# Performance work log

Measured on AMD Instinct MI355X. Metric: run time of the kernel, lower is better.

The kernel has to match this reference:

```python
import jax, jax.numpy as jnp
import numpy as np

DIM, N_HEAD, N_KV, HEAD_DIM = 4096, 32, 8, 128
B, S = 2, 2048


def apply_rotary_emb(x, freqs_cis):
    # x: [B, S, H, D]; freqs_cis: [S, D//2, 2]
    xs = x.reshape(x.shape[:-1] + (-1, 2))            # [B,S,H,D/2,2]
    f = freqs_cis.reshape(1, xs.shape[1], 1, xs.shape[3], 2)
    x0, x1 = xs[..., 0], xs[..., 1]
    f0, f1 = f[..., 0], f[..., 1]
    out = jnp.stack([x0 * f0 - x1 * f1, x0 * f1 + x1 * f0], axis=-1)
    return out.reshape(x.shape).astype(x.dtype)


def setup_inputs() -> dict:
    key = jax.random.key(0)
    k1, k2, k3, k4 = jax.random.split(key, 4)
    x = jax.random.normal(k1, (B, S, DIM), dtype=jnp.float32)
    freqs_cis = jax.random.normal(k2, (S, HEAD_DIM // 2, 2), dtype=jnp.float32)
    # causal boolean mask (True = attend)
    mask_cache = jnp.tril(jnp.ones((S, S), dtype=bool))[None, None]
    input_pos = jnp.arange(S, dtype=jnp.int32)
    total_head_dim = (N_HEAD + 2 * N_KV) * HEAD_DIM
    wqkv = jax.random.normal(k3, (total_head_dim, DIM), dtype=jnp.float32) * (DIM ** -0.5)
    wo = jax.random.normal(k4, (DIM, DIM), dtype=jnp.float32) * (DIM ** -0.5)
    return {"x": x, "freqs_cis": freqs_cis, "mask_cache": mask_cache,
            "input_pos": input_pos, "wqkv": wqkv, "wo": wo}


def reference(x, freqs_cis, mask_cache, input_pos, wqkv, wo):
    bsz, seqlen, _ = x.shape
    kv_size = N_KV * HEAD_DIM
    qkv = jnp.einsum('bsd,fd->bsf', x, wqkv)
    q, k, v = jnp.split(qkv, [DIM, DIM + kv_size], axis=-1)
    q = q.reshape(bsz, seqlen, N_HEAD, HEAD_DIM)
    k = k.reshape(bsz, seqlen, N_KV, HEAD_DIM)
    v = v.reshape(bsz, seqlen, N_KV, HEAD_DIM)
    q = apply_rotary_emb(q, freqs_cis)
    k = apply_rotary_emb(k, freqs_cis)
    q = q.transpose(0, 2, 1, 3)   # [B,Hq,S,D]
    k = k.transpose(0, 2, 1, 3)   # [B,Hkv,S,D]
    v = v.transpose(0, 2, 1, 3)
    # GQA: repeat kv heads to match query heads
    g = N_HEAD // N_KV
    k = jnp.repeat(k, g, axis=1)
    v = jnp.repeat(v, g, axis=1)
    scale = 1.0 / jnp.sqrt(jnp.asarray(HEAD_DIM, dtype=q.dtype))
    scores = jnp.einsum('bhqd,bhkd->bhqk', q, k) * scale
    neg_inf = jnp.asarray(jnp.finfo(scores.dtype).min, dtype=scores.dtype)
    scores = jnp.where(mask_cache, scores, neg_inf)
    attn = jax.nn.softmax(scores, axis=-1)
    y = jnp.einsum('bhqk,bhkd->bhqd', attn, v)
    y = y.transpose(0, 2, 1, 3).reshape(bsz, seqlen, DIM)
    return jnp.einsum('bsd,od->bso', y, wo)
```

## Files before the change

kernel.cpp:

```cpp
#include <hip/hip_runtime.h>
#include <hip/hip_bf16.h>

#define DIM   4096
#define NHEAD 32
#define NKV   8
#define HD    128
#define BATCH 2
#define SEQ   2048
#define M1    (BATCH*SEQ)
#define NF    ((NHEAD+2*NKV)*HD)

typedef __attribute__((ext_vector_type(8))) short short8;
typedef __attribute__((ext_vector_type(4))) short short4v;
typedef __attribute__((ext_vector_type(4))) float f32x4;

__device__ __forceinline__ float bf2f(short s) {
    unsigned u = ((unsigned)(unsigned short)s) << 16;
    return __builtin_bit_cast(float, u);
}
__device__ __forceinline__ short f2bf(float f) {
    unsigned u = __builtin_bit_cast(unsigned, f);
    u = u + 0x7fffu + ((u >> 16) & 1u);
    return (short)(u >> 16);
}

__device__ __forceinline__ void gload_lds16(const void* g, void* l) {
    __builtin_amdgcn_global_load_lds(
        (const __attribute__((address_space(1))) void*)g,
        (__attribute__((address_space(3))) void*)l, 16, 0, 0);
}

__global__ void f2bf2_k(const float* __restrict__ a, short* __restrict__ da, int na8,
                        const float* __restrict__ b, short* __restrict__ db, int nb8) {
    const int total = na8 + nb8;
    const int stride = gridDim.x * blockDim.x;
    for (int i = blockIdx.x * blockDim.x + threadIdx.x; i < total; i += stride) {
        const float* s; short* d; int j = i;
        if (j < na8) { s = a; d = da; }
        else         { j -= na8; s = b; d = db; }
        float4 v0 = ((const float4*)s)[2*j];
        float4 v1 = ((const float4*)s)[2*j + 1];
        short8 o;
        o[0] = f2bf(v0.x); o[1] = f2bf(v0.y); o[2] = f2bf(v0.z); o[3] = f2bf(v0.w);
        o[4] = f2bf(v1.x); o[5] = f2bf(v1.y); o[6] = f2bf(v1.z); o[7] = f2bf(v1.w);
        ((short8*)d)[j] = o;
    }
}
__global__ void f2bf_k(const float* __restrict__ src, short* __restrict__ dst, int n8) {
    const int stride = gridDim.x * blockDim.x;
    for (int i = blockIdx.x * blockDim.x + threadIdx.x; i < n8; i += stride) {
        float4 v0 = ((const float4*)src)[2*i];
        float4 v1 = ((const float4*)src)[2*i + 1];
        short8 o;
        o[0] = f2bf(v0.x); o[1] = f2bf(v0.y); o[2] = f2bf(v0.z); o[3] = f2bf(v0.w);
        o[4] = f2bf(v1.x); o[5] = f2bf(v1.y); o[6] = f2bf(v1.z); o[7] = f2bf(v1.w);
        ((short8*)dst)[i] = o;
    }
}

template<int OUT_BF16>
__global__ __launch_bounds__(512, 2) void gemm256(const short* __restrict__ A,
                                                  const short* __restrict__ Bm,
                                                  void* __restrict__ Cout,
                                                  int M, int N, int K) {
    __shared__ __align__(16) short As[2][2][128*64];
    __shared__ __align__(16) short Bs[2][2][128*64];
    const int nbn = N >> 8;
    const int nwg = gridDim.x;
    const int cpx = nwg >> 3;
    const int swz = (blockIdx.x & 7) * cpx + (blockIdx.x >> 3);
    const int brow = swz / nbn, bcol = swz % nbn;
    const int t = threadIdx.x, lane = t & 63, w = t >> 6;
    const int wm = w >> 2, wn = w & 3;
    const int l16 = lane & 15, lhi = lane >> 4, l7 = l16 & 7;
    const size_t abase = (size_t)brow * 256 * K;
    const size_t bbase = (size_t)bcol * 256 * K;
    const int sr = t >> 3;
    const int sc = t & 7;
    const int scl = sc ^ (sr & 7);
    f32x4 acc[8][4] = {};

    auto stageA = [&](int kt, int qm) {
#pragma unroll
        for (int i = 0; i < 2; ++i)
            gload_lds16(A + abase + (size_t)(i*128 + qm*64 + sr) * K + kt*64 + scl*8,
                        &As[kt & 1][qm][(i*64 + sr)*64 + sc*8]);
    };
    auto stageB = [&](int kt, int qn) {
#pragma unroll
        for (int i = 0; i < 2; ++i)
            gload_lds16(Bm + bbase + (size_t)((i*2 + (sr>>5))*64 + qn*32 + (sr & 31)) * K + kt*64 + scl*8,
                        &Bs[kt & 1][qn][(i*64 + sr)*64 + sc*8]);
    };

    const int NT = K >> 6;
    stageA(0, 0); stageB(0, 0); stageA(0, 1); stageB(0, 1);
    stageA(1, 0); stageB(1, 0);
    asm volatile("s_waitcnt vmcnt(4)" ::: "memory");
    __builtin_amdgcn_s_barrier();

    short8 a0[4][2], a1[4][2], b0[2][2], b1[2][2];

#define LD_A(dst, P, QM)                                                        \
    _Pragma("unroll") for (int mi = 0; mi < 4; ++mi)                            \
    _Pragma("unroll") for (int kk = 0; kk < 2; ++kk)                            \
        dst[mi][kk] = *(const short8*)&As[P][QM][(wm*64 + mi*16 + l16)*64 + (((kk*4 + lhi) ^ l7) * 8)];
#define LD_B(dst, P, QN)                                                        \
    _Pragma("unroll") for (int ni = 0; ni < 2; ++ni)                            \
    _Pragma("unroll") for (int kk = 0; kk < 2; ++kk)                            \
        dst[ni][kk] = *(const short8*)&Bs[P][QN][(wn*32 + ni*16 + l16)*64 + (((kk*4 + lhi) ^ l7) * 8)];
#define MMA(QM, QN, af, bf)                                                     \
    __builtin_amdgcn_s_barrier();                                               \
    __builtin_amdgcn_s_setprio(1);                                              \
    _Pragma("unroll") for (int kk = 0; kk < 2; ++kk)                            \
    _Pragma("unroll") for (int mi = 0; mi < 4; ++mi)                            \
    _Pragma("unroll") for (int ni = 0; ni < 2; ++ni)                            \
        acc[QM*4 + mi][QN*2 + ni] = __builtin_amdgcn_mfma_f32_16x16x32_bf16(    \
            af[mi][kk], bf[ni][kk], acc[QM*4 + mi][QN*2 + ni], 0, 0, 0);        \
    __builtin_amdgcn_s_setprio(0);

    LD_A(a0, 0, 0)
    LD_B(b0, 0, 0)

    for (int cur = 0; cur < NT; ++cur) {
        const int d = cur & 1, dn = d ^ 1;
        LD_B(b1, d, 1)
        if (cur + 1 < NT) stageA(cur + 1, 1);
        MMA(0, 0, a0, b0)
        asm volatile("s_waitcnt vmcnt(2)" ::: "memory");
        LD_A(a1, d, 1)
        if (cur + 1 < NT) stageB(cur + 1, 1);
        MMA(0, 1, a0, b1)
        LD_A(a0, dn, 0)
        if (cur + 2 < NT) stageA(cur + 2, 0);
        MMA(1, 0, a1, b0)
        if (cur + 2 < NT) { asm volatile("s_waitcnt vmcnt(2)" ::: "memory"); }
        else              { asm volatile("s_waitcnt vmcnt(0)" ::: "memory"); }
        LD_B(b0, dn, 0)
        if (cur + 2 < NT) stageB(cur + 2, 0);
        MMA(1, 1, a1, b1)
    }
#undef LD_A
#undef LD_B
#undef MMA

#pragma unroll
    for (int fm = 0; fm < 8; ++fm)
#pragma unroll
        for (int fn = 0; fn < 4; ++fn)
#pragma unroll
            for (int r = 0; r < 4; ++r) {
                size_t row = (size_t)brow*256 + wm*128 + fm*16 + lhi*4 + r;
                size_t col = (size_t)bcol*256 + wn*64 + fn*16 + l16;
                if (OUT_BF16)
                    ((short*)Cout)[row * N + col] = f2bf(acc[fm][fn][r]);
                else
                    ((float*)Cout)[row * N + col] = acc[fm][fn][r];
            }
}

__global__ void rope_split_k(const short* __restrict__ qkv,
                             const float* __restrict__ freqs,
                             short* __restrict__ qb, short* __restrict__ kb) {
    int tid  = blockIdx.x * blockDim.x + threadIdx.x;
    int colg = tid % 640;
    int row  = tid / 640;
    if (row >= M1) return;
    int b = row >> 11, s = row & 2047;
    int f = colg << 3;
    int h = f >> 7, d = f & 127;
    short8 v = *(const short8*)&qkv[(size_t)row * NF + f];
    const float4 fa = *(const float4*)&freqs[(size_t)(s*64 + (d>>1)) * 2];
    const float4 fb = *(const float4*)&freqs[(size_t)(s*64 + (d>>1)) * 2 + 4];
    float fr[8] = {fa.x, fa.y, fa.z, fa.w, fb.x, fb.y, fb.z, fb.w};
    short8 o;
#pragma unroll
    for (int p = 0; p < 4; ++p) {
        float x0 = bf2f(v[2*p]), x1 = bf2f(v[2*p+1]);
        float c = fr[2*p], sn = fr[2*p+1];
        o[2*p]   = f2bf(x0 * c  - x1 * sn);
        o[2*p+1] = f2bf(x0 * sn + x1 * c);
    }
    if (h < NHEAD)
        *(short8*)&qb[((((size_t)b*NHEAD + h)*SEQ + s) << 7) + d] = o;
    else
        *(short8*)&kb[((((size_t)b*NKV + (h - NHEAD))*SEQ + s) << 7) + d] = o;
}

__global__ __launch_bounds__(256) void vrepack_k(const short* __restrict__ qkv,
                                                 short* __restrict__ vg) {
    __shared__ short Ls[32][130];
    const int bid = blockIdx.x;
    const int st = bid & 63, kv = (bid >> 6) & 7, b = bid >> 9;
    const int t = threadIdx.x;
    const int dcol = (t & 15) * 8, sl = t >> 4;
#pragma unroll
    for (int p = 0; p < 2; ++p) {
        int s = p*16 + sl;
        short8 v = *(const short8*)&qkv[(size_t)(b*2048 + st*32 + s)*NF + 5120 + kv*128 + dcol];
#pragma unroll
        for (int j = 0; j < 8; ++j) Ls[s][dcol + j] = v[j];
    }
    __syncthreads();
    size_t base = (((size_t)b*NKV + kv) << 18) + st*4096;
#pragma unroll
    for (int p = 0; p < 2; ++p) {
        int c = p*256 + t;
        short8 o;
#pragma unroll
        for (int j = 0; j < 8; ++j) o[j] = Ls[(c & 3)*8 + j][c >> 2];
        *(short8*)&vg[base + c*8] = o;
    }
}

__global__ __launch_bounds__(256, 3) void attn_k(const short* __restrict__ qb_,
                                                 const short* __restrict__ kb_,
                                                 const short* __restrict__ vg_,
                                                 short* __restrict__ yb) {
    __shared__ __align__(16) short Ks[2][32*128];
    __shared__ __align__(16) short Vs[2][128*32];
    __shared__ __align__(16) short Pw[4][32*36];
    const int bid = blockIdx.x;
    const int qt = 15 - (bid >> 6);
    const int bh = bid & 63;
    const int b = bh >> 5, h = bh & 31, kv = h >> 2;
    const int t = threadIdx.x, lane = t & 63, w = t >> 6;
    const int l16 = lane & 15, lhi = lane >> 4;
    const short* Qp = qb_ + (((size_t)(b*NHEAD + h)*SEQ + qt*128 + w*32) << 7);
    const short* Kp = kb_ + (((size_t)(b*NKV + kv)*SEQ) << 7);
    const short* Vp = vg_ + (((size_t)(b*NKV + kv)*SEQ) << 7);
    short8 qf[2][4];
#pragma unroll
    for (int qq = 0; qq < 2; ++qq)
#pragma unroll
        for (int kk = 0; kk < 4; ++kk)
            qf[qq][kk] = *(const short8*)&Qp[(qq*16 + l16)*HD + kk*32 + lhi*8];
    f32x4 oacc[2][8] = {};
    float mrow[2] = {-1e30f, -1e30f};
    float lsum[2] = {0.f, 0.f};
    const int NT = (qt + 1) * 4;
    const int qmaxw = qt*128 + w*32 + 31;
    const float sc = 0.08838834764831845f;

    auto stage = [&](int kt, int buf) {
#pragma unroll
        for (int i = 0; i < 2; ++i) {
            int L = i*256 + t;
            int r = L >> 4, s = L & 15;
            int gs = (s & 8) | ((s & 7) ^ (r & 7));
            gload_lds16(Kp + (size_t)kt*4096 + r*128 + gs*8, &Ks[buf][L*8]);
        }
#pragma unroll
        for (int i = 0; i < 2; ++i) {
            int L = i*256 + t;
            int r8 = L >> 3, s3 = L & 7;
            int gs = s3 ^ (r8 & 7);
            gload_lds16(Vp + (size_t)kt*4096 + (r8*8 + gs)*8, &Vs[buf][L*8]);
        }
    };

    stage(0, 0);
    __syncthreads();
    int cur = 0;
    for (int kt = 0; kt < NT; ++kt) {
        if (kt + 1 < NT) stage(kt + 1, cur ^ 1);
        if (kt*32 <= qmaxw) {
            f32x4 sT[2][2] = {};
#pragma unroll
            for (int kk = 0; kk < 4; ++kk) {
                short8 kf[2];
#pragma unroll
                for (int kb2 = 0; kb2 < 2; ++kb2) {
                    int row = kb2*16 + l16;
                    int ch  = kk*4 + lhi;
                    int chs = (ch & 8) | ((ch & 7) ^ (row & 7));
                    kf[kb2] = *(const short8*)&Ks[cur][row*128 + chs*8];
                }
#pragma unroll
                for (int kb2 = 0; kb2 < 2; ++kb2)
#pragma unroll
                    for (int qq = 0; qq < 2; ++qq)
                        sT[kb2][qq] = __builtin_amdgcn_mfma_f32_16x16x32_bf16(kf[kb2], qf[qq][kk], sT[kb2][qq], 0, 0, 0);
            }
#pragma unroll
            for (int qq = 0; qq < 2; ++qq) {
                int qg = qt*128 + w*32 + qq*16 + l16;
                float tmax = -1e30f;
#pragma unroll
                for (int kb2 = 0; kb2 < 2; ++kb2)
#pragma unroll
                    for (int r = 0; r < 4; ++r) {
                        int kg = kt*32 + kb2*16 + lhi*4 + r;
                        float sv = sT[kb2][qq][r] * sc;
                        sv = (kg > qg) ? -1e30f : sv;
                        sT[kb2][qq][r] = sv;
                        tmax = fmaxf(tmax, sv);
                    }
                tmax = fmaxf(tmax, __shfl_xor(tmax, 16, 64));
                tmax = fmaxf(tmax, __shfl_xor(tmax, 32, 64));
                float mn = fmaxf(mrow[qq], tmax);
                float alpha = __expf(mrow[qq] - mn);
                mrow[qq] = mn;
                float rsum = 0.f;
#pragma unroll
                for (int kb2 = 0; kb2 < 2; ++kb2) {
                    short4v pk;
#pragma unroll
                    for (int r = 0; r < 4; ++r) {
                        float p = __expf(sT[kb2][qq][r] - mn);
                        rsum += p;
                        pk[r] = f2bf(p);
                    }
                    *(short4v*)&Pw[w][(qq*16 + l16)*36 + kb2*16 + lhi*4] = pk;
                }
                rsum += __shfl_xor(rsum, 16, 64);
                rsum += __shfl_xor(rsum, 32, 64);
                lsum[qq] = lsum[qq]*alpha + rsum;
                float a4[4];
#pragma unroll
                for (int r = 0; r < 4; ++r)
                    a4[r] = __shfl(alpha, (lane & 48) | (lhi*4 + r), 64);
#pragma unroll
                for (int n = 0; n < 8; ++n)
#pragma unroll
                    for (int r = 0; r < 4; ++r)
                        oacc[qq][n][r] *= a4[r];
            }
            short8 pf[2];
#pragma unroll
            for (int qq = 0; qq < 2; ++qq)
                pf[qq] = *(const short8*)&Pw[w][(qq*16 + l16)*36 + lhi*8];
#pragma unroll
            for (int n = 0; n < 8; ++n) {
                int d   = n*16 + l16;
                int lch = d*4 + lhi;
                int phys = (lch & ~7) | ((lch & 7) ^ ((lch >> 3) & 7));
                short8 vf = *(const short8*)&Vs[cur][phys*8];
#pragma unroll
                for (int qq = 0; qq < 2; ++qq)
                    oacc[qq][n] = __builtin_amdgcn_mfma_f32_16x16x32_bf16(pf[qq], vf, oacc[qq][n], 0, 0, 0);
            }
        }
        __syncthreads();
        cur ^= 1;
    }
#pragma unroll
    for (int qq = 0; qq < 2; ++qq) {
        float inv = 1.f / lsum[qq];
        float i4[4];
#pragma unroll
        for (int r = 0; r < 4; ++r)
            i4[r] = __shfl(inv, (lane & 48) | (lhi*4 + r), 64);
#pragma unroll
        for (int n = 0; n < 8; ++n)
#pragma unroll
            for (int r = 0; r < 4; ++r) {
                size_t row = (size_t)b*SEQ + qt*128 + w*32 + qq*16 + lhi*4 + r;
                yb[row*DIM + h*HD + n*16 + l16] = f2bf(oacc[qq][n][r] * i4[r]);
            }
    }
}

extern "C" void kernel_launch(void* const* d_in, const int* in_sizes, int n_in,
                              void* d_out, int out_size, void* d_ws, size_t ws_size,
                              hipStream_t stream) {
    const float* x     = (const float*)d_in[0];
    const float* freqs = (const float*)d_in[1];
    const float* wqkv  = (const float*)d_in[4];
    const float* wo    = (const float*)d_in[5];
    float* out = (float*)d_out;
    char* ws = (char*)d_ws;
    const size_t MB = 1024*1024;
    short* xb    = (short*)ws;
    short* yb    = (short*)ws;
    short* wqkvb = (short*)(ws + 32*MB);
    short* wob   = (short*)(ws + 32*MB);
    short* qkvb  = (short*)(ws + 80*MB);
    short* qb    = (short*)(ws + 128*MB);
    short* kb    = (short*)(ws + 160*MB);
    short* vg    = (short*)(ws + 168*MB);

    const int na8 = DIM*DIM/8, nb8 = NF*DIM/8;
    f2bf2_k<<<2048, 256, 0, stream>>>(x, xb, na8, wqkv, wqkvb, nb8);
    gemm256<1><<<(M1/256)*(NF/256), 512, 0, stream>>>(xb, wqkvb, qkvb, M1, NF, DIM);
    rope_split_k<<<(M1*640)/256, 256, 0, stream>>>(qkvb, freqs, qb, kb);
    vrepack_k<<<BATCH*NKV*(SEQ/32), 256, 0, stream>>>(qkvb, vg);
    attn_k<<<BATCH*NHEAD*(SEQ/128), 256, 0, stream>>>(qb, kb, vg, yb);
    f2bf_k<<<2048, 256, 0, stream>>>(wo, wob, DIM*DIM/8);
    gemm256<0><<<(M1/256)*(DIM/256), 512, 0, stream>>>(yb, wob, out, M1, DIM, DIM);
}
```

Before: 516.3 us.

## Merge prep launches, overlap wo conversion with attention, add lazy softmax rescale

Merges the RoPE/split kernel and the V repack kernel into one launch, branching on block index. Appends 64 extra blocks to the attention grid that convert wo to bf16, so that work can fill idle CUs during the causal-attention tail instead of running as a separate launch. Inside attention, it raises wave priority around the MFMA sections. It also skips the online-softmax rescale of the output accumulator when no new row max exceeds the running max by more than 8, which saves the shuffles and multiplies at the cost of unnormalised exponentials up to e^8 in the P values.

```diff
diff --git a/kernel.cpp b/kernel.cpp
--- a/kernel.cpp
+++ b/kernel.cpp
@@ -44,17 +44,6 @@
         o[0] = f2bf(v0.x); o[1] = f2bf(v0.y); o[2] = f2bf(v0.z); o[3] = f2bf(v0.w);
         o[4] = f2bf(v1.x); o[5] = f2bf(v1.y); o[6] = f2bf(v1.z); o[7] = f2bf(v1.w);
         ((short8*)d)[j] = o;
-    }
-}
-__global__ void f2bf_k(const float* __restrict__ src, short* __restrict__ dst, int n8) {
-    const int stride = gridDim.x * blockDim.x;
-    for (int i = blockIdx.x * blockDim.x + threadIdx.x; i < n8; i += stride) {
-        float4 v0 = ((const float4*)src)[2*i];
-        float4 v1 = ((const float4*)src)[2*i + 1];
-        short8 o;
-        o[0] = f2bf(v0.x); o[1] = f2bf(v0.y); o[2] = f2bf(v0.z); o[3] = f2bf(v0.w);
-        o[4] = f2bf(v1.x); o[5] = f2bf(v1.y); o[6] = f2bf(v1.z); o[7] = f2bf(v1.w);
-        ((short8*)dst)[i] = o;
     }
 }
 
@@ -159,72 +148,89 @@
             }
 }
 
-__global__ void rope_split_k(const short* __restrict__ qkv,
-                             const float* __restrict__ freqs,
-                             short* __restrict__ qb, short* __restrict__ kb) {
-    int tid  = blockIdx.x * blockDim.x + threadIdx.x;
-    int colg = tid % 640;
-    int row  = tid / 640;
-    if (row >= M1) return;
-    int b = row >> 11, s = row & 2047;
-    int f = colg << 3;
-    int h = f >> 7, d = f & 127;
-    short8 v = *(const short8*)&qkv[(size_t)row * NF + f];
-    const float4 fa = *(const float4*)&freqs[(size_t)(s*64 + (d>>1)) * 2];
-    const float4 fb = *(const float4*)&freqs[(size_t)(s*64 + (d>>1)) * 2 + 4];
-    float fr[8] = {fa.x, fa.y, fa.z, fa.w, fb.x, fb.y, fb.z, fb.w};
-    short8 o;
-#pragma unroll
-    for (int p = 0; p < 4; ++p) {
-        float x0 = bf2f(v[2*p]), x1 = bf2f(v[2*p+1]);
-        float c = fr[2*p], sn = fr[2*p+1];
-        o[2*p]   = f2bf(x0 * c  - x1 * sn);
-        o[2*p+1] = f2bf(x0 * sn + x1 * c);
-    }
-    if (h < NHEAD)
-        *(short8*)&qb[((((size_t)b*NHEAD + h)*SEQ + s) << 7) + d] = o;
-    else
-        *(short8*)&kb[((((size_t)b*NKV + (h - NHEAD))*SEQ + s) << 7) + d] = o;
-}
-
-__global__ __launch_bounds__(256) void vrepack_k(const short* __restrict__ qkv,
-                                                 short* __restrict__ vg) {
+#define ROPE_BLKS (M1*640/256)
+__global__ __launch_bounds__(256) void prep_k(const short* __restrict__ qkv,
+                                              const float* __restrict__ freqs,
+                                              short* __restrict__ qb,
+                                              short* __restrict__ kb,
+                                              short* __restrict__ vg) {
     __shared__ short Ls[32][130];
-    const int bid = blockIdx.x;
-    const int st = bid & 63, kv = (bid >> 6) & 7, b = bid >> 9;
     const int t = threadIdx.x;
-    const int dcol = (t & 15) * 8, sl = t >> 4;
-#pragma unroll
-    for (int p = 0; p < 2; ++p) {
-        int s = p*16 + sl;
-        short8 v = *(const short8*)&qkv[(size_t)(b*2048 + st*32 + s)*NF + 5120 + kv*128 + dcol];
-#pragma unroll
-        for (int j = 0; j < 8; ++j) Ls[s][dcol + j] = v[j];
-    }
-    __syncthreads();
-    size_t base = (((size_t)b*NKV + kv) << 18) + st*4096;
-#pragma unroll
-    for (int p = 0; p < 2; ++p) {
-        int c = p*256 + t;
+    if (blockIdx.x < ROPE_BLKS) {
+        int tid  = blockIdx.x * 256 + t;
+        int colg = tid % 640;
+        int row  = tid / 640;
+        int b = row >> 11, s = row & 2047;
+        int f = colg << 3;
+        int h = f >> 7, d = f & 127;
+        short8 v = *(const short8*)&qkv[(size_t)row * NF + f];
+        const float4 fa = *(const float4*)&freqs[(size_t)(s*64 + (d>>1)) * 2];
+        const float4 fb = *(const float4*)&freqs[(size_t)(s*64 + (d>>1)) * 2 + 4];
+        float fr[8] = {fa.x, fa.y, fa.z, fa.w, fb.x, fb.y, fb.z, fb.w};
         short8 o;
 #pragma unroll
-        for (int j = 0; j < 8; ++j) o[j] = Ls[(c & 3)*8 + j][c >> 2];
-        *(short8*)&vg[base + c*8] = o;
-    }
-}
-
+        for (int p = 0; p < 4; ++p) {
+            float x0 = bf2f(v[2*p]), x1 = bf2f(v[2*p+1]);
+            float c = fr[2*p], sn = fr[2*p+1];
+            o[2*p]   = f2bf(x0 * c  - x1 * sn);
+            o[2*p+1] = f2bf(x0 * sn + x1 * c);
+        }
+        if (h < NHEAD)
+            *(short8*)&qb[((((size_t)b*NHEAD + h)*SEQ + s) << 7) + d] = o;
+        else
+            *(short8*)&kb[((((size_t)b*NKV + (h - NHEAD))*SEQ + s) << 7) + d] = o;
+    } else {
+        const int bid = blockIdx.x - ROPE_BLKS;
+        const int st = bid & 63, kv = (bid >> 6) & 7, b = bid >> 9;
+        const int dcol = (t & 15) * 8, sl = t >> 4;
+#pragma unroll
+        for (int p = 0; p < 2; ++p) {
+            int s = p*16 + sl;
+            short8 v = *(const short8*)&qkv[(size_t)(b*2048 + st*32 + s)*NF + 5120 + kv*128 + dcol];
+#pragma unroll
+            for (int j = 0; j < 8; ++j) Ls[s][dcol + j] = v[j];
+        }
+        __syncthreads();
+        size_t base = (((size_t)b*NKV + kv) << 18) + st*4096;
+#pragma unroll
+        for (int p = 0; p < 2; ++p) {
+            int c = p*256 + t;
+            short8 o;
+#pragma unroll
+            for (int j = 0; j < 8; ++j) o[j] = Ls[(c & 3)*8 + j][c >> 2];
+            *(short8*)&vg[base + c*8] = o;
+        }
+    }
+}
+
+#define ATTN_BLKS (BATCH*NHEAD*(SEQ/128))
 __global__ __launch_bounds__(256, 3) void attn_k(const short* __restrict__ qb_,
                                                  const short* __restrict__ kb_,
                                                  const short* __restrict__ vg_,
-                                                 short* __restrict__ yb) {
+                                                 short* __restrict__ yb,
+                                                 const float* __restrict__ wo,
+                                                 short* __restrict__ wob) {
     __shared__ __align__(16) short Ks[2][32*128];
     __shared__ __align__(16) short Vs[2][128*32];
     __shared__ __align__(16) short Pw[4][32*36];
     const int bid = blockIdx.x;
+    const int t = threadIdx.x;
+    if (bid >= ATTN_BLKS) {
+        const int stride = 64 * 256;
+        for (int i = (bid - ATTN_BLKS)*256 + t; i < DIM*DIM/8; i += stride) {
+            float4 v0 = ((const float4*)wo)[2*i];
+            float4 v1 = ((const float4*)wo)[2*i + 1];
+            short8 o;
+            o[0] = f2bf(v0.x); o[1] = f2bf(v0.y); o[2] = f2bf(v0.z); o[3] = f2bf(v0.w);
+            o[4] = f2bf(v1.x); o[5] = f2bf(v1.y); o[6] = f2bf(v1.z); o[7] = f2bf(v1.w);
+            ((short8*)wob)[i] = o;
+        }
+        return;
+    }
     const int qt = 15 - (bid >> 6);
     const int bh = bid & 63;
     const int b = bh >> 5, h = bh & 31, kv = h >> 2;
-    const int t = threadIdx.x, lane = t & 63, w = t >> 6;
+    const int lane = t & 63, w = t >> 6;
     const int l16 = lane & 15, lhi = lane >> 4;
     const short* Qp = qb_ + (((size_t)(b*NHEAD + h)*SEQ + qt*128 + w*32) << 7);
     const short* Kp = kb_ + (((size_t)(b*NKV + kv)*SEQ) << 7);
@@ -266,6 +272,7 @@
         if (kt + 1 < NT) stage(kt + 1, cur ^ 1);
         if (kt*32 <= qmaxw) {
             f32x4 sT[2][2] = {};
+            __builtin_amdgcn_s_setprio(1);
 #pragma unroll
             for (int kk = 0; kk < 4; ++kk) {
                 short8 kf[2];
@@ -282,6 +289,7 @@
                     for (int qq = 0; qq < 2; ++qq)
                         sT[kb2][qq] = __builtin_amdgcn_mfma_f32_16x16x32_bf16(kf[kb2], qf[qq][kk], sT[kb2][qq], 0, 0, 0);
             }
+            __builtin_amdgcn_s_setprio(0);
 #pragma unroll
             for (int qq = 0; qq < 2; ++qq) {
                 int qg = qt*128 + w*32 + qq*16 + l16;
@@ -298,9 +306,14 @@
                     }
                 tmax = fmaxf(tmax, __shfl_xor(tmax, 16, 64));
                 tmax = fmaxf(tmax, __shfl_xor(tmax, 32, 64));
-                float mn = fmaxf(mrow[qq], tmax);
-                float alpha = __expf(mrow[qq] - mn);
-                mrow[qq] = mn;
+                float mn, alpha;
+                bool noresc = __all(tmax <= mrow[qq] + 8.0f);
+                if (noresc) { mn = mrow[qq]; alpha = 1.0f; }
+                else {
+                    mn = fmaxf(mrow[qq], tmax);
+                    alpha = __expf(mrow[qq] - mn);
+                    mrow[qq] = mn;
+                }
                 float rsum = 0.f;
 #pragma unroll
                 for (int kb2 = 0; kb2 < 2; ++kb2) {
@@ -315,21 +328,26 @@
                 }
                 rsum += __shfl_xor(rsum, 16, 64);
                 rsum += __shfl_xor(rsum, 32, 64);
-                lsum[qq] = lsum[qq]*alpha + rsum;
-                float a4[4];
-#pragma unroll
-                for (int r = 0; r < 4; ++r)
-                    a4[r] = __shfl(alpha, (lane & 48) | (lhi*4 + r), 64);
-#pragma unroll
-                for (int n = 0; n < 8; ++n)
+                if (noresc) {
+                    lsum[qq] += rsum;
+                } else {
+                    lsum[qq] = lsum[qq]*alpha + rsum;
+                    float a4[4];
 #pragma unroll
                     for (int r = 0; r < 4; ++r)
-                        oacc[qq][n][r] *= a4[r];
+                        a4[r] = __shfl(alpha, (lane & 48) | (lhi*4 + r), 64);
+#pragma unroll
+                    for (int n = 0; n < 8; ++n)
+#pragma unroll
+                        for (int r = 0; r < 4; ++r)
+                            oacc[qq][n][r] *= a4[r];
+                }
             }
             short8 pf[2];
 #pragma unroll
             for (int qq = 0; qq < 2; ++qq)
                 pf[qq] = *(const short8*)&Pw[w][(qq*16 + l16)*36 + lhi*8];
+            __builtin_amdgcn_s_setprio(1);
 #pragma unroll
             for (int n = 0; n < 8; ++n) {
                 int d   = n*16 + l16;
@@ -340,6 +358,7 @@
                 for (int qq = 0; qq < 2; ++qq)
                     oacc[qq][n] = __builtin_amdgcn_mfma_f32_16x16x32_bf16(pf[qq], vf, oacc[qq][n], 0, 0, 0);
             }
+            __builtin_amdgcn_s_setprio(0);
         }
         __syncthreads();
         cur ^= 1;
@@ -383,9 +402,7 @@
     const int na8 = DIM*DIM/8, nb8 = NF*DIM/8;
     f2bf2_k<<<2048, 256, 0, stream>>>(x, xb, na8, wqkv, wqkvb, nb8);
     gemm256<1><<<(M1/256)*(NF/256), 512, 0, stream>>>(xb, wqkvb, qkvb, M1, NF, DIM);
-    rope_split_k<<<(M1*640)/256, 256, 0, stream>>>(qkvb, freqs, qb, kb);
-    vrepack_k<<<BATCH*NKV*(SEQ/32), 256, 0, stream>>>(qkvb, vg);
-    attn_k<<<BATCH*NHEAD*(SEQ/128), 256, 0, stream>>>(qb, kb, vg, yb);
-    f2bf_k<<<2048, 256, 0, stream>>>(wo, wob, DIM*DIM/8);
+    prep_k<<<ROPE_BLKS + BATCH*NKV*(SEQ/32), 256, 0, stream>>>(qkvb, freqs, qb, kb, vg);
+    attn_k<<<ATTN_BLKS + 64, 256, 0, stream>>>(qb, kb, vg, yb, wo, wob);
     gemm256<0><<<(M1/256)*(DIM/256), 512, 0, stream>>>(yb, wob, out, M1, DIM, DIM);
 }
```

New measurement: 538.7 us. 4.3% more time.
